# Performance work log

Hardware: AMD Instinct MI355X
Metric: run time of the kernel (lower is better)

The kernel has to match this reference:

```python
import jax, jax.numpy as jnp
import numpy as np

# BlendParams defaults (pytorch3d)
SIGMA = 1e-4
GAMMA = 1e-4
BG_BLUE = 1.0       # background_color = (1,1,1); module returns channel 2
ZNEAR = 1.0
ZFAR = 100.0
EPS = 1e-10

N, H, W, K = 8, 256, 256, 50


def setup_inputs() -> dict:
    key = jax.random.key(0)
    k1, k2, k3 = jax.random.split(key, 3)
    # depth buffer values in [znear, zfar]
    zbuf = jax.random.uniform(k1, (N, H, W, K), dtype=jnp.float32) * (ZFAR - ZNEAR) + ZNEAR
    # signed (squared) pixel-to-edge distances: small magnitudes near 0
    dists = jax.random.normal(k2, (N, H, W, K), dtype=jnp.float32) * 1e-3
    # face indices; -1 marks empty slots (~1/100000 here, plus explicit tail masking)
    pix_to_face = jax.random.randint(k3, (N, H, W, K), -1, 100000, dtype=jnp.int64)
    # make the last few K-slots empty, as a real rasterizer would
    slot = jnp.arange(K)
    pix_to_face = jnp.where(slot < K - 5, pix_to_face, jnp.int64(-1))
    return {"zbuf": zbuf, "dists": dists, "pix_to_face": pix_to_face}


def reference(zbuf, dists, pix_to_face):
    # softmax_rgb_blend with colors == zbuf broadcast over 3 channels;
    # the module returns images[..., 2] (blue channel of the blended RGBA).
    mask = (pix_to_face >= 0).astype(zbuf.dtype)                      # (N,H,W,K)
    prob = jax.nn.sigmoid(-dists / SIGMA) * mask                      # distance sigmoid
    # z-based softmax weights (stabilized by per-pixel max)
    z_inv = (ZFAR - zbuf) / (ZFAR - ZNEAR) * mask                     # (N,H,W,K)
    z_inv_max = jnp.maximum(jnp.max(z_inv, axis=-1, keepdims=True), EPS)
    weights_num = prob * jnp.exp((z_inv - z_inv_max) / GAMMA)         # (N,H,W,K)
    delta = jnp.maximum(jnp.exp((EPS - z_inv_max) / GAMMA), EPS)      # (N,H,W,1)
    denom = jnp.sum(weights_num, axis=-1, keepdims=True) + delta      # (N,H,W,1)
    # weighted color sum; all three channels equal zbuf, take channel 2
    weighted = jnp.sum(weights_num * zbuf, axis=-1, keepdims=True)    # (N,H,W,1)
    blue = (weighted + delta * BG_BLUE) / denom                       # (N,H,W,1)
    return blue[..., 0]                                               # (N,H,W)
```

## Files before the change

### kernel.cpp

```cpp
#include <hip/hip_runtime.h>


constexpr int THREADS = 256;
constexpr int LPP     = 8;
constexpr int TPB     = THREADS / LPP;

constexpr float INV_SIGMA  = 1e4f;
constexpr float INVG       = 1e4f;
constexpr float ZFAR       = 100.0f;
constexpr float ZRANGE     = 99.0f;
constexpr float INV_ZRANGE = 1.0f / 99.0f;
constexpr float EPS        = 1e-10f;

__device__ __forceinline__ void pixel_blend(
    const int2 fa, const int2 fb, const int2 fc, const int2 fd,
    const float2 za, const float2 zb, const float2 zc, const float2 zd,
    const float2 da, const float2 db, const float2 dc, const float2 dd,
    const bool tail_owner,
    float& m_out, float& s1_out, float& s2_out)
{
    const bool m0 = (fa.x >= 0),               m1 = (fa.y >= 0);
    const bool m2 = (fb.x >= 0),               m3 = (fb.y >= 0);
    const bool m4 = (fc.x >= 0),               m5 = (fc.y >= 0);
    const bool m6 = tail_owner && (fd.x >= 0), m7 = tail_owner && (fd.y >= 0);

    float zv[8], pv[8];
    zv[0] = m0 ? (ZFAR - za.x) * INV_ZRANGE : 0.0f;
    zv[1] = m1 ? (ZFAR - za.y) * INV_ZRANGE : 0.0f;
    zv[2] = m2 ? (ZFAR - zb.x) * INV_ZRANGE : 0.0f;
    zv[3] = m3 ? (ZFAR - zb.y) * INV_ZRANGE : 0.0f;
    zv[4] = m4 ? (ZFAR - zc.x) * INV_ZRANGE : 0.0f;
    zv[5] = m5 ? (ZFAR - zc.y) * INV_ZRANGE : 0.0f;
    zv[6] = m6 ? (ZFAR - zd.x) * INV_ZRANGE : 0.0f;
    zv[7] = m7 ? (ZFAR - zd.y) * INV_ZRANGE : 0.0f;
    pv[0] = m0 ? 1.0f / (1.0f + __expf(da.x * INV_SIGMA)) : 0.0f;
    pv[1] = m1 ? 1.0f / (1.0f + __expf(da.y * INV_SIGMA)) : 0.0f;
    pv[2] = m2 ? 1.0f / (1.0f + __expf(db.x * INV_SIGMA)) : 0.0f;
    pv[3] = m3 ? 1.0f / (1.0f + __expf(db.y * INV_SIGMA)) : 0.0f;
    pv[4] = m4 ? 1.0f / (1.0f + __expf(dc.x * INV_SIGMA)) : 0.0f;
    pv[5] = m5 ? 1.0f / (1.0f + __expf(dc.y * INV_SIGMA)) : 0.0f;
    pv[6] = m6 ? 1.0f / (1.0f + __expf(dd.x * INV_SIGMA)) : 0.0f;
    pv[7] = m7 ? 1.0f / (1.0f + __expf(dd.y * INV_SIGMA)) : 0.0f;

    float m = fmaxf(fmaxf(fmaxf(zv[0], zv[1]), fmaxf(zv[2], zv[3])),
                    fmaxf(fmaxf(zv[4], zv[5]), fmaxf(zv[6], zv[7])));
    m = fmaxf(m, __shfl_xor(m, 1));
    m = fmaxf(m, __shfl_xor(m, 2));
    m = fmaxf(m, __shfl_xor(m, 4));
    m = fmaxf(m, EPS);

    float S1a = 0.0f, S1b = 0.0f, S2a = 0.0f, S2b = 0.0f;
    #pragma unroll
    for (int j = 0; j < 8; j += 2) {
        const float w0 = pv[j]   * __expf((zv[j]   - m) * INVG);
        const float w1 = pv[j+1] * __expf((zv[j+1] - m) * INVG);
        S1a += w0;
        S1b += w1;
        S2a += w0 * (ZFAR - zv[j]   * ZRANGE);
        S2b += w1 * (ZFAR - zv[j+1] * ZRANGE);
    }
    float S1 = S1a + S1b;
    float S2 = S2a + S2b;
    S1 += __shfl_xor(S1, 1);  S1 += __shfl_xor(S1, 2);  S1 += __shfl_xor(S1, 4);
    S2 += __shfl_xor(S2, 1);  S2 += __shfl_xor(S2, 2);  S2 += __shfl_xor(S2, 4);

    m_out = m;  s1_out = S1;  s2_out = S2;
}

__global__ __launch_bounds__(THREADS, 4) void soft_depth_kernel(
    const float* __restrict__ zbuf,
    const float* __restrict__ dists,
    const int*   __restrict__ p2f,
    float*       __restrict__ out)
{
    const int t = threadIdx.x;
    const int q = t & (LPP - 1);
    const size_t team = (size_t)blockIdx.x * TPB + (t >> 3);
    const size_t pix0 = 2 * team;
    const size_t cbA  = pix0 * 25;
    const size_t cbB  = cbA + 25;

    const float2* __restrict__ z2 = (const float2*)zbuf;
    const float2* __restrict__ d2 = (const float2*)dists;
    const int2*   __restrict__ f2 = (const int2*)p2f;

    const size_t a0 = cbA + q, a1 = cbA + q + 8, a2 = cbA + q + 16, a3 = cbA + 24;
    const size_t b0 = cbB + q, b1 = cbB + q + 8, b2 = cbB + q + 16, b3 = cbB + 24;

    const int2   fA0 = f2[a0], fA1 = f2[a1], fA2 = f2[a2], fA3 = f2[a3];
    const int2   fB0 = f2[b0], fB1 = f2[b1], fB2 = f2[b2], fB3 = f2[b3];
    const float2 zA0 = z2[a0], zA1 = z2[a1], zA2 = z2[a2], zA3 = z2[a3];
    const float2 zB0 = z2[b0], zB1 = z2[b1], zB2 = z2[b2], zB3 = z2[b3];
    const float2 dA0 = d2[a0], dA1 = d2[a1], dA2 = d2[a2], dA3 = d2[a3];
    const float2 dB0 = d2[b0], dB1 = d2[b1], dB2 = d2[b2], dB3 = d2[b3];
    __builtin_amdgcn_sched_barrier(0);

    const bool town = (q == 0);
    float mA, S1A, S2A, mB, S1B, S2B;
    pixel_blend(fA0, fA1, fA2, fA3, zA0, zA1, zA2, zA3,
                dA0, dA1, dA2, dA3, town, mA, S1A, S2A);
    pixel_blend(fB0, fB1, fB2, fB3, zB0, zB1, zB2, zB3,
                dB0, dB1, dB2, dB3, town, mB, S1B, S2B);

    if (q < 2) {
        const float m  = (q == 0) ? mA  : mB;
        const float s1 = (q == 0) ? S1A : S1B;
        const float s2 = (q == 0) ? S2A : S2B;
        const float delta = fmaxf(__expf((EPS - m) * INVG), EPS);
        out[pix0 + (size_t)q] = (s2 + delta) / (s1 + delta);
    }
}

extern "C" void kernel_launch(void* const* d_in, const int* in_sizes, int n_in,
                              void* d_out, int out_size, void* d_ws, size_t ws_size,
                              hipStream_t stream) {
    const float* zbuf  = (const float*)d_in[0];
    const float* dists = (const float*)d_in[1];
    const int*   p2f   = (const int*)d_in[2];
    float* out = (float*)d_out;

    const int pixels = out_size;
    const int teams  = pixels / 2;
    const int blocks = teams / TPB;

    soft_depth_kernel<<<dim3(blocks), dim3(THREADS), 0, stream>>>(
        zbuf, dists, p2f, out);
}
```

Before: 284.9 us.

## Stream tiles through double-buffered LDS with global_load_lds in persistent blocks

Replaces the one-shot direct global loads with a persistent grid of 256 blocks of 512 threads. Each block walks a contiguous range of 128-pixel tiles and prefetches the next tile's zbuf, dists and face-index data into a second LDS buffer using direct global-to-LDS 16-byte loads while it computes on the current buffer. The aim is to overlap memory traffic with compute and to make global reads fully coalesced. In exchange, occupancy is limited to one large block per CU with about 150KB of LDS, a full vmcnt(0) wait plus a barrier after every tile, and reads from LDS with an 8-byte stride.

```diff
diff --git a/kernel.cpp b/kernel.cpp
--- a/kernel.cpp
+++ b/kernel.cpp
@@ -1,9 +1,15 @@
 #include <hip/hip_runtime.h>
 
 
-constexpr int THREADS = 256;
-constexpr int LPP     = 8;
-constexpr int TPB     = THREADS / LPP;
+constexpr int THREADS = 512;
+constexpr int WAVES   = THREADS / 64;
+constexpr int TILE_PX = 128;
+constexpr int PX_B    = 200;
+constexpr int ARR_B   = TILE_PX * PX_B;
+constexpr int BUF_B   = 3 * ARR_B;
+constexpr int ASTEPS  = ARR_B / 1024;
+constexpr int STEPS   = 3 * ASTEPS;
+constexpr int NBLOCKS = 256;
 
 constexpr float INV_SIGMA  = 1e4f;
 constexpr float INVG       = 1e4f;
@@ -11,6 +17,10 @@
 constexpr float ZRANGE     = 99.0f;
 constexpr float INV_ZRANGE = 1.0f / 99.0f;
 constexpr float EPS        = 1e-10f;
+
+#define GLDS16(gp, lp) __builtin_amdgcn_global_load_lds(                     \
+    (const __attribute__((address_space(1))) void*)(gp),                     \
+    (__attribute__((address_space(3))) void*)(lp), 16, 0, 0)
 
 __device__ __forceinline__ void pixel_blend(
     const int2 fa, const int2 fb, const int2 fc, const int2 fd,
@@ -67,47 +77,89 @@
     m_out = m;  s1_out = S1;  s2_out = S2;
 }
 
-__global__ __launch_bounds__(THREADS, 4) void soft_depth_kernel(
+__global__ __launch_bounds__(THREADS, 1) void soft_depth_kernel(
     const float* __restrict__ zbuf,
     const float* __restrict__ dists,
     const int*   __restrict__ p2f,
-    float*       __restrict__ out)
+    float*       __restrict__ out,
+    const int tiles_per_block)
 {
-    const int t = threadIdx.x;
-    const int q = t & (LPP - 1);
-    const size_t team = (size_t)blockIdx.x * TPB + (t >> 3);
-    const size_t pix0 = 2 * team;
-    const size_t cbA  = pix0 * 25;
-    const size_t cbB  = cbA + 25;
+    __shared__ __align__(16) char smem[2 * BUF_B];
 
-    const float2* __restrict__ z2 = (const float2*)zbuf;
-    const float2* __restrict__ d2 = (const float2*)dists;
-    const int2*   __restrict__ f2 = (const int2*)p2f;
+    const int t    = threadIdx.x;
+    const int lane = t & 63;
+    const int wid  = t >> 6;
+    const int q    = t & 7;
+    const int team = t >> 3;
 
-    const size_t a0 = cbA + q, a1 = cbA + q + 8, a2 = cbA + q + 16, a3 = cbA + 24;
-    const size_t b0 = cbB + q, b1 = cbB + q + 8, b2 = cbB + q + 16, b3 = cbB + 24;
+    const char* __restrict__ zc = (const char*)zbuf;
+    const char* __restrict__ dc = (const char*)dists;
+    const char* __restrict__ fc = (const char*)p2f;
 
-    const int2   fA0 = f2[a0], fA1 = f2[a1], fA2 = f2[a2], fA3 = f2[a3];
-    const int2   fB0 = f2[b0], fB1 = f2[b1], fB2 = f2[b2], fB3 = f2[b3];
-    const float2 zA0 = z2[a0], zA1 = z2[a1], zA2 = z2[a2], zA3 = z2[a3];
-    const float2 zB0 = z2[b0], zB1 = z2[b1], zB2 = z2[b2], zB3 = z2[b3];
-    const float2 dA0 = d2[a0], dA1 = d2[a1], dA2 = d2[a2], dA3 = d2[a3];
-    const float2 dB0 = d2[b0], dB1 = d2[b1], dB2 = d2[b2], dB3 = d2[b3];
+    const int tile0 = blockIdx.x * tiles_per_block;
+
+    auto stage = [&](int tile, char* buf) {
+        const size_t tb = (size_t)tile * ARR_B;
+        const char* zt = zc + tb;
+        const char* dt = dc + tb;
+        const char* ft = fc + tb;
+        for (int s = wid; s < STEPS; s += WAVES) {
+            const int a = s / ASTEPS;
+            const int j = s - a * ASTEPS;
+            const char* g = (a == 0) ? zt : (a == 1) ? dt : ft;
+            GLDS16(g + j * 1024 + lane * 16, buf + a * ARR_B + j * 1024);
+        }
+    };
+
+    auto compute = [&](int tile, const char* buf) {
+        const float2* __restrict__ zl = (const float2*)(buf);
+        const float2* __restrict__ dl = (const float2*)(buf + ARR_B);
+        const int2*   __restrict__ fl = (const int2*)(buf + 2 * ARR_B);
+
+        const int pA  = 2 * team;
+        const int cbA = pA * 25;
+        const int cbB = cbA + 25;
+        const int a0 = cbA + q, a1 = cbA + q + 8, a2 = cbA + q + 16, a3 = cbA + 24;
+        const int b0 = cbB + q, b1 = cbB + q + 8, b2 = cbB + q + 16, b3 = cbB + 24;
+
+        const int2   fA0 = fl[a0], fA1 = fl[a1], fA2 = fl[a2], fA3 = fl[a3];
+        const int2   fB0 = fl[b0], fB1 = fl[b1], fB2 = fl[b2], fB3 = fl[b3];
+        const float2 zA0 = zl[a0], zA1 = zl[a1], zA2 = zl[a2], zA3 = zl[a3];
+        const float2 zB0 = zl[b0], zB1 = zl[b1], zB2 = zl[b2], zB3 = zl[b3];
+        const float2 dA0 = dl[a0], dA1 = dl[a1], dA2 = dl[a2], dA3 = dl[a3];
+        const float2 dB0 = dl[b0], dB1 = dl[b1], dB2 = dl[b2], dB3 = dl[b3];
+
+        const bool town = (q == 0);
+        float mA, S1A, S2A, mB, S1B, S2B;
+        pixel_blend(fA0, fA1, fA2, fA3, zA0, zA1, zA2, zA3,
+                    dA0, dA1, dA2, dA3, town, mA, S1A, S2A);
+        pixel_blend(fB0, fB1, fB2, fB3, zB0, zB1, zB2, zB3,
+                    dB0, dB1, dB2, dB3, town, mB, S1B, S2B);
+
+        if (q < 2) {
+            const float m  = (q == 0) ? mA  : mB;
+            const float s1 = (q == 0) ? S1A : S1B;
+            const float s2 = (q == 0) ? S2A : S2B;
+            const float delta = fmaxf(__expf((EPS - m) * INVG), EPS);
+            out[(size_t)tile * TILE_PX + pA + q] = (s2 + delta) / (s1 + delta);
+        }
+    };
+
+    int cur = 0;
+    stage(tile0, smem);
+    asm volatile("s_waitcnt vmcnt(0)" ::: "memory");
+    __builtin_amdgcn_s_barrier();
     __builtin_amdgcn_sched_barrier(0);
 
-    const bool town = (q == 0);
-    float mA, S1A, S2A, mB, S1B, S2B;
-    pixel_blend(fA0, fA1, fA2, fA3, zA0, zA1, zA2, zA3,
-                dA0, dA1, dA2, dA3, town, mA, S1A, S2A);
-    pixel_blend(fB0, fB1, fB2, fB3, zB0, zB1, zB2, zB3,
-                dB0, dB1, dB2, dB3, town, mB, S1B, S2B);
-
-    if (q < 2) {
-        const float m  = (q == 0) ? mA  : mB;
-        const float s1 = (q == 0) ? S1A : S1B;
-        const float s2 = (q == 0) ? S2A : S2B;
-        const float delta = fmaxf(__expf((EPS - m) * INVG), EPS);
-        out[pix0 + (size_t)q] = (s2 + delta) / (s1 + delta);
+    for (int i = 0; i < tiles_per_block; ++i) {
+        if (i + 1 < tiles_per_block)
+            stage(tile0 + i + 1, smem + (cur ^ 1) * BUF_B);
+        __builtin_amdgcn_sched_barrier(0);
+        compute(tile0 + i, smem + cur * BUF_B);
+        asm volatile("s_waitcnt vmcnt(0)" ::: "memory");
+        __builtin_amdgcn_s_barrier();
+        __builtin_amdgcn_sched_barrier(0);
+        cur ^= 1;
     }
 }
 
@@ -120,9 +172,9 @@
     float* out = (float*)d_out;
 
     const int pixels = out_size;
-    const int teams  = pixels / 2;
-    const int blocks = teams / TPB;
+    const int tiles  = pixels / TILE_PX;
+    const int tpb    = tiles / NBLOCKS;
 
-    soft_depth_kernel<<<dim3(blocks), dim3(THREADS), 0, stream>>>(
-        zbuf, dists, p2f, out);
+    soft_depth_kernel<<<dim3(NBLOCKS), dim3(THREADS), 0, stream>>>(
+        zbuf, dists, p2f, out, tpb);
 }
```

Measured after the change: 298.6 us. 4.8% more time.
